# Kernel tuning notes

Measured on AMD Instinct MI355X. Metric: run time of the kernel, lower is better.

The kernel has to match this reference:

```python
import jax, jax.numpy as jnp
import numpy as np
import math

D_MODEL = 1024
N_HEADS = 16
HEAD_DIM = D_MODEL // N_HEADS


def setup_inputs() -> dict:
    key = jax.random.key(0)
    ks = jax.random.split(key, 6)
    scale = 1.0 / math.sqrt(D_MODEL)
    x = jax.random.normal(ks[0], (4, 2048, D_MODEL), dtype=jnp.float32)
    # nn.Linear weights stored as [out, in]; we keep [in, out] for x @ W
    Wq = jax.random.uniform(ks[1], (D_MODEL, D_MODEL), jnp.float32, -scale, scale)
    Wk = jax.random.uniform(ks[2], (D_MODEL, D_MODEL), jnp.float32, -scale, scale)
    Wv = jax.random.uniform(ks[3], (D_MODEL, D_MODEL), jnp.float32, -scale, scale)
    Wo = jax.random.uniform(ks[4], (D_MODEL, D_MODEL), jnp.float32, -scale, scale)
    bo = jax.random.uniform(ks[5], (D_MODEL,), jnp.float32, -scale, scale)
    return {"x": x, "Wq": Wq, "Wk": Wk, "Wv": Wv, "Wo": Wo, "bo": bo}


def reference(x, Wq, Wk, Wv, Wo, bo):
    B, S, _ = x.shape
    H, Dh = N_HEADS, HEAD_DIM
    # project and split heads -> [B, H, S, Dh]
    q = (x @ Wq).reshape(B, S, H, Dh).transpose(0, 2, 1, 3)
    k = (x @ Wk).reshape(B, S, H, Dh).transpose(0, 2, 1, 3)
    v = (x @ Wv).reshape(B, S, H, Dh).transpose(0, 2, 1, 3)
    scores = jnp.einsum('bhqd,bhkd->bhqk', q, k) / math.sqrt(Dh)
    causal = jnp.tril(jnp.ones((S, S), dtype=bool))  # True = keep
    scores = jnp.where(causal, scores, -jnp.inf)
    attn = jax.nn.softmax(scores, axis=-1)  # dropout=0.0 -> no-op
    out = jnp.einsum('bhqk,bhkd->bhqd', attn, v)
    out = out.transpose(0, 2, 1, 3).reshape(B, S, H * Dh)
    return out @ Wo + bo
```

## Files before the change

kernel.cpp:

```cpp
#include <hip/hip_runtime.h>
#include <hip/hip_bf16.h>

#define DEV __device__ __forceinline__

typedef unsigned short u16;
typedef unsigned int u32;
typedef __bf16 bf16x8 __attribute__((ext_vector_type(8)));
typedef float f32x4 __attribute__((ext_vector_type(4)));

static constexpr int S   = 2048;
static constexpr int D   = 1024;
static constexpr int H   = 16;
static constexpr int Dh  = 64;
static constexpr int B_  = 4;
static constexpr int M   = B_ * S;

DEV u16 f2bf(float f) {
    __hip_bfloat16 h = __float2bfloat16(f);
    union { __hip_bfloat16 h; u16 u; } cv; cv.h = h; return cv.u;
}
DEV float bf2f(u16 u) {
    union { u16 u; __hip_bfloat16 h; } cv; cv.u = u; return __bfloat162float(cv.h);
}
DEV f32x4 mfma16(bf16x8 a, bf16x8 b, f32x4 c) {
    return __builtin_amdgcn_mfma_f32_16x16x32_bf16(a, b, c, 0, 0, 0);
}
DEV void llds16(const u16* g, u16* l) {
    __builtin_amdgcn_global_load_lds(
        (const __attribute__((address_space(1))) u32*)g,
        (__attribute__((address_space(3))) u32*)l, 16, 0, 0);
}
DEV bf16x8 ld8f(const float* p) {
    const f32x4* q = reinterpret_cast<const f32x4*>(p);
    f32x4 a = q[0], b = q[1];
    union { u16 u[8]; bf16x8 v; } r;
    r.u[0] = f2bf(a[0]); r.u[1] = f2bf(a[1]); r.u[2] = f2bf(a[2]); r.u[3] = f2bf(a[3]);
    r.u[4] = f2bf(b[0]); r.u[5] = f2bf(b[1]); r.u[6] = f2bf(b[2]); r.u[7] = f2bf(b[3]);
    return r.v;
}

__global__ __launch_bounds__(256) void x_to_bf16(
    const float* __restrict__ x, u16* __restrict__ xb)
{
    size_t i = ((size_t)blockIdx.x * 256 + threadIdx.x) * 8;
    *reinterpret_cast<bf16x8*>(xb + i) = ld8f(x + i);
}

__global__ __launch_bounds__(256) void transpose_w(
    const float* __restrict__ Wq, const float* __restrict__ Wk,
    const float* __restrict__ Wv, const float* __restrict__ Wo,
    u16* __restrict__ WT)
{
    const float* src = blockIdx.z == 0 ? Wq : blockIdx.z == 1 ? Wk
                     : blockIdx.z == 2 ? Wv : Wo;
    u16* dst = WT + (size_t)blockIdx.z * D * D;
    __shared__ u16 T[64 * 72];
    const int k0 = blockIdx.x * 64, n0 = blockIdx.y * 64;
    const int tid = threadIdx.x;
    for (int c = tid; c < 512; c += 256) {
        int r = c >> 3, cc = (c & 7) << 3;
        *reinterpret_cast<bf16x8*>(&T[r * 72 + cc]) =
            ld8f(&src[(size_t)(k0 + r) * D + n0 + cc]);
    }
    __syncthreads();
    for (int c = tid; c < 512; c += 256) {
        int r = c >> 3, cc = (c & 7) << 3;
        u16 tmp[8];
        #pragma unroll
        for (int i = 0; i < 8; ++i) tmp[i] = T[(cc + i) * 72 + r];
        *reinterpret_cast<bf16x8*>(&dst[(size_t)(n0 + r) * D + k0 + cc]) =
            *reinterpret_cast<const bf16x8*>(tmp);
    }
}

__global__ __launch_bounds__(256) void qkv_gemm128(
    const u16* __restrict__ A, const u16* __restrict__ WT,
    u16* __restrict__ qkv, u16* __restrict__ vtb)
{
    const int bm = blockIdx.x;
    const int bn = blockIdx.y;

    __shared__ u16 As[128 * 32];
    __shared__ u16 Bs[128 * 32];
    __shared__ u16 Tt[64 * 136];

    const int tid  = threadIdx.x;
    const int wave = tid >> 6, ln = tid & 63;
    const int ln15 = ln & 15, quad = ln >> 4;
    const int wm = (wave >> 1) * 64, wn = (wave & 1) * 64;

    const u16* Ab = A  + (size_t)(bm * 128) * D;
    const u16* Bb = WT + (size_t)(bn * 128) * D;

    const int c0  = wave * 128 + ln;
    const int c1  = c0 + 64;
    const int r0  = c0 >> 2, o0 = (c0 & 3) * 8;
    const int r1  = c1 >> 2, o1 = (c1 & 3) * 8;

    f32x4 acc[4][4] = {};

    for (int k0 = 0; k0 < D; k0 += 32) {
        __syncthreads();
        llds16(Ab + (size_t)r0 * D + k0 + o0, &As[(wave * 2 + 0) * 512]);
        llds16(Ab + (size_t)r1 * D + k0 + o1, &As[(wave * 2 + 1) * 512]);
        llds16(Bb + (size_t)r0 * D + k0 + o0, &Bs[(wave * 2 + 0) * 512]);
        llds16(Bb + (size_t)r1 * D + k0 + o1, &Bs[(wave * 2 + 1) * 512]);
        __syncthreads();
        bf16x8 af[4], bfr[4];
        #pragma unroll
        for (int i = 0; i < 4; ++i)
            af[i] = *reinterpret_cast<const bf16x8*>(&As[(wm + i * 16 + ln15) * 32 + quad * 8]);
        #pragma unroll
        for (int j = 0; j < 4; ++j)
            bfr[j] = *reinterpret_cast<const bf16x8*>(&Bs[(wn + j * 16 + ln15) * 32 + quad * 8]);
        #pragma unroll
        for (int i = 0; i < 4; ++i)
            #pragma unroll
            for (int j = 0; j < 4; ++j)
                acc[i][j] = mfma16(af[i], bfr[j], acc[i][j]);
    }

    const int matn = bn >> 3;
    if (matn < 2) {
        u16* outp = qkv + (size_t)matn * M * D;
        #pragma unroll
        for (int i = 0; i < 4; ++i)
            #pragma unroll
            for (int j = 0; j < 4; ++j)
                #pragma unroll
                for (int r = 0; r < 4; ++r) {
                    int t = bm * 128 + wm + i * 16 + quad * 4 + r;
                    int b = t >> 11, s = t & (S - 1);
                    int n = (bn & 7) * 128 + wn + j * 16 + ln15;
                    int head = n >> 6, dh = n & 63;
                    outp[(((size_t)(b * H + head)) * S + s) * Dh + dh] = f2bf(acc[i][j][r]);
                }
    } else {
        const int t0 = bm * 128, b = t0 >> 11, s0 = t0 & (S - 1);
        #pragma unroll
        for (int h2 = 0; h2 < 2; ++h2) {
            __syncthreads();
            if ((wn == 0) == (h2 == 0)) {
                #pragma unroll
                for (int i = 0; i < 4; ++i)
                    #pragma unroll
                    for (int j = 0; j < 4; ++j)
                        #pragma unroll
                        for (int r = 0; r < 4; ++r) {
                            int sl = wm + i * 16 + quad * 4 + r;
                            int dh = j * 16 + ln15;
                            Tt[dh * 136 + sl] = f2bf(acc[i][j][r]);
                        }
            }
            __syncthreads();
            const int bh = b * H + (bn & 7) * 2 + h2;
            u16* dst = vtb + (size_t)bh * Dh * S + s0;
            for (int c = tid; c < 1024; c += 256) {
                int r = c >> 4, cc = (c & 15) * 8;
                *reinterpret_cast<bf16x8*>(&dst[(size_t)r * S + cc]) =
                    *reinterpret_cast<const bf16x8*>(&Tt[r * 136 + cc]);
            }
        }
    }
}

__global__ __launch_bounds__(256) void attn_kernel(
    const u16* __restrict__ qbuf, const u16* __restrict__ kbuf,
    const u16* __restrict__ vt, u16* __restrict__ attno)
{
    const int i  = blockIdx.x;
    const int bh = blockIdx.y;
    const int b = bh >> 4, h = bh & 15;
    const int qt[4] = {i, 15 - i, 16 + i, 31 - i};

    __shared__ u16 Ks[2][64 * 64];
    __shared__ u16 Vs[2][64 * 64];
    __shared__ u16 Ps[4][16 * 72];

    const int tid  = threadIdx.x;
    const int wave = tid >> 6, ln = tid & 63;
    const int ln15 = ln & 15, quad = ln >> 4;
    const int swz  = ln15 & 7;

    const u16* kp0 = kbuf + (size_t)bh * S * Dh;
    const u16* vp0 = vt   + (size_t)bh * Dh * S;

    bf16x8 qf[4][2];
    #pragma unroll
    for (int t = 0; t < 4; ++t) {
        const u16* qp = qbuf + ((size_t)bh * S + qt[t] * 64) * Dh;
        for (int c = tid; c < 512; c += 256) {
            int r = c >> 3, cc = (c & 7) << 3;
            *reinterpret_cast<bf16x8*>(&Ks[0][r * 64 + cc]) =
                *reinterpret_cast<const bf16x8*>(&qp[r * 64 + cc]);
        }
        __syncthreads();
        #pragma unroll
        for (int st = 0; st < 2; ++st) {
            union { bf16x8 v; u16 u[8]; } in, ot;
            in.v = *reinterpret_cast<const bf16x8*>(&Ks[0][(wave * 16 + ln15) * 64 + st * 32 + quad * 8]);
            #pragma unroll
            for (int k = 0; k < 8; ++k) ot.u[k] = f2bf(bf2f(in.u[k]) * 0.18033688f);
            qf[t][st] = ot.v;
        }
        __syncthreads();
    }

    float l_st[4][4] = {};
    f32x4 o_st[4][4] = {};

    u16* psw = &Ps[wave][0];
    const int lrow = wave * 16 + quad * 4;

    const int c0 = wave * 128 + ln;
    const int c1 = c0 + 64;
    const int kr0 = c0 >> 3, ko0 = (((c0 & 7) ^ (kr0 & 7)) * 8);
    const int kr1 = c1 >> 3, ko1 = (((c1 & 7) ^ (kr1 & 7)) * 8);

    auto stage = [&](int kblk, int buf) {
        llds16(kp0 + ((size_t)kblk * 64 + kr0) * Dh + ko0, &Ks[buf][(wave * 2 + 0) * 512]);
        llds16(kp0 + ((size_t)kblk * 64 + kr1) * Dh + ko1, &Ks[buf][(wave * 2 + 1) * 512]);
        llds16(vp0 + (size_t)kr0 * S + kblk * 64 + ko0,    &Vs[buf][(wave * 2 + 0) * 512]);
        llds16(vp0 + (size_t)kr1 * S + kblk * 64 + ko1,    &Vs[buf][(wave * 2 + 1) * 512]);
    };

    bf16x8 kf[2][4], vf[2][4];

    auto step = [&](int t, bool domask) {
        const bf16x8* qa = qf[t];
        float* l_r = l_st[t];
        f32x4* oa = o_st[t];
        f32x4 sf[4] = {};
        #pragma unroll
        for (int j = 0; j < 4; ++j) {
            sf[j] = mfma16(qa[0], kf[0][j], sf[j]);
            sf[j] = mfma16(qa[1], kf[1][j], sf[j]);
        }
        if (domask) {
            #pragma unroll
            for (int j = 0; j < 4; ++j) {
                int kg = j * 16 + ln15;
                #pragma unroll
                for (int r = 0; r < 4; ++r)
                    if (kg > lrow + r) sf[j][r] = -3e38f;
            }
        }
        #pragma unroll
        for (int j = 0; j < 4; ++j)
            #pragma unroll
            for (int r = 0; r < 4; ++r) {
                float p = exp2f(sf[j][r] - 24.0f);
                sf[j][r] = p;
                l_r[r] += p;
            }
        #pragma unroll
        for (int j = 0; j < 4; ++j)
            #pragma unroll
            for (int r = 0; r < 4; ++r)
                psw[(quad * 4 + r) * 72 + j * 16 + ln15] = f2bf(sf[j][r]);

        #pragma unroll
        for (int st = 0; st < 2; ++st) {
            bf16x8 pa = *reinterpret_cast<const bf16x8*>(&psw[ln15 * 72 + st * 32 + quad * 8]);
            #pragma unroll
            for (int jd = 0; jd < 4; ++jd)
                oa[jd] = mfma16(pa, vf[st][jd], oa[jd]);
        }
    };

    const int nstage = qt[3] + 1;
    stage(0, 0);
    int cur = 0;
    for (int kblk = 0; kblk < nstage; ++kblk) {
        __syncthreads();
        if (kblk + 1 < nstage) stage(kblk + 1, cur ^ 1);
        #pragma unroll
        for (int st = 0; st < 2; ++st)
            #pragma unroll
            for (int j = 0; j < 4; ++j) {
                kf[st][j] = *reinterpret_cast<const bf16x8*>(
                    &Ks[cur][(j * 16 + ln15) * 64 + ((st * 4 + quad) ^ swz) * 8]);
                vf[st][j] = *reinterpret_cast<const bf16x8*>(
                    &Vs[cur][(j * 16 + ln15) * 64 + ((st * 4 + quad) ^ swz) * 8]);
            }
        step(3, kblk == qt[3]);
        if (kblk <= qt[2]) step(2, kblk == qt[2]);
        if (kblk <= qt[1]) step(1, kblk == qt[1]);
        if (kblk <= qt[0]) step(0, kblk == qt[0]);
        cur ^= 1;
    }

    #pragma unroll
    for (int t = 0; t < 4; ++t) {
        float linv[4];
        #pragma unroll
        for (int r = 0; r < 4; ++r) {
            float l = l_st[t][r];
            l += __shfl_xor(l, 1, 64);
            l += __shfl_xor(l, 2, 64);
            l += __shfl_xor(l, 4, 64);
            l += __shfl_xor(l, 8, 64);
            linv[r] = 1.0f / l;
        }
        #pragma unroll
        for (int jd = 0; jd < 4; ++jd)
            #pragma unroll
            for (int r = 0; r < 4; ++r) {
                int qrow = qt[t] * 64 + wave * 16 + quad * 4 + r;
                size_t off = ((size_t)(b * S + qrow)) * D + h * Dh + jd * 16 + ln15;
                attno[off] = f2bf(o_st[t][jd][r] * linv[r]);
            }
    }
}

__global__ __launch_bounds__(256) void proj_gemm128(
    const u16* __restrict__ A, const u16* __restrict__ WoT,
    const float* __restrict__ bo, float* __restrict__ out)
{
    const int bm = blockIdx.x;
    const int bn = blockIdx.y;

    __shared__ u16 As[128 * 32];
    __shared__ u16 Bs[128 * 32];

    const int tid  = threadIdx.x;
    const int wave = tid >> 6, ln = tid & 63;
    const int ln15 = ln & 15, quad = ln >> 4;
    const int wm = (wave >> 1) * 64, wn = (wave & 1) * 64;

    const u16* Ab = A   + (size_t)(bm * 128) * D;
    const u16* Bb = WoT + (size_t)(bn * 128) * D;

    const int c0 = wave * 128 + ln;
    const int c1 = c0 + 64;
    const int r0 = c0 >> 2, o0 = (c0 & 3) * 8;
    const int r1 = c1 >> 2, o1 = (c1 & 3) * 8;

    f32x4 acc[4][4] = {};

    for (int k0 = 0; k0 < D; k0 += 32) {
        __syncthreads();
        llds16(Ab + (size_t)r0 * D + k0 + o0, &As[(wave * 2 + 0) * 512]);
        llds16(Ab + (size_t)r1 * D + k0 + o1, &As[(wave * 2 + 1) * 512]);
        llds16(Bb + (size_t)r0 * D + k0 + o0, &Bs[(wave * 2 + 0) * 512]);
        llds16(Bb + (size_t)r1 * D + k0 + o1, &Bs[(wave * 2 + 1) * 512]);
        __syncthreads();
        bf16x8 af[4], bfr[4];
        #pragma unroll
        for (int i = 0; i < 4; ++i)
            af[i] = *reinterpret_cast<const bf16x8*>(&As[(wm + i * 16 + ln15) * 32 + quad * 8]);
        #pragma unroll
        for (int j = 0; j < 4; ++j)
            bfr[j] = *reinterpret_cast<const bf16x8*>(&Bs[(wn + j * 16 + ln15) * 32 + quad * 8]);
        #pragma unroll
        for (int i = 0; i < 4; ++i)
            #pragma unroll
            for (int j = 0; j < 4; ++j)
                acc[i][j] = mfma16(af[i], bfr[j], acc[i][j]);
    }

    #pragma unroll
    for (int i = 0; i < 4; ++i)
        #pragma unroll
        for (int j = 0; j < 4; ++j)
            #pragma unroll
            for (int r = 0; r < 4; ++r) {
                int t   = bm * 128 + wm + i * 16 + quad * 4 + r;
                int col = bn * 128 + wn + j * 16 + ln15;
                out[(size_t)t * D + col] = acc[i][j][r] + bo[col];
            }
}

extern "C" void kernel_launch(void* const* d_in, const int* in_sizes, int n_in,
                              void* d_out, int out_size, void* d_ws, size_t ws_size,
                              hipStream_t stream) {
    const float* x  = (const float*)d_in[0];
    const float* Wq = (const float*)d_in[1];
    const float* Wk = (const float*)d_in[2];
    const float* Wv = (const float*)d_in[3];
    const float* Wo = (const float*)d_in[4];
    const float* bo = (const float*)d_in[5];
    float* out = (float*)d_out;
    u16* ws  = (u16*)d_ws;

    u16* WT   = ws;
    u16* xb   = WT + (size_t)4 * D * D;
    u16* qkvb = xb + (size_t)M * D;
    u16* kb   = qkvb + (size_t)M * D;
    u16* vtb  = qkvb + (size_t)2 * M * D;
    u16* attn = xb;

    x_to_bf16   <<<dim3(M * D / (256 * 8)), 256, 0, stream>>>(x, xb);
    transpose_w <<<dim3(16, 16, 4), 256, 0, stream>>>(Wq, Wk, Wv, Wo, WT);
    qkv_gemm128 <<<dim3(64, 24),    256, 0, stream>>>(xb, WT, qkvb, vtb);
    attn_kernel <<<dim3(8, 64),     256, 0, stream>>>(qkvb, kb, vtb, attn);
    proj_gemm128<<<dim3(64, 8),     256, 0, stream>>>(attn, WT + (size_t)3 * D * D, bo, out);
}
```

Baseline: 280.3 us.

## Split attention into two query tiles per block and stage Q/K stores via LDS

The attention kernel now gives each block two paired query tiles (i, 31-i) instead of four, which doubles the grid to 16x64 blocks for more parallelism and fewer registers per thread. The constant softmax offset is folded into the MFMA accumulator initial value, and the P tile in shared memory switches to an XOR-swizzled layout with no padding to avoid bank conflicts. In the QKV GEMM, Q/K outputs are staged through a shared LDS buffer so they can be written to global memory as vectorized 16-byte stores instead of scattered 2-byte stores, and the LDS arrays are aliased to cut shared memory use. In exchange, K/V tiles are loaded from global memory twice as often across blocks, and the GEMM epilogue needs extra barriers.

Measured after the change: 288.4 us. 2.9% more time.

```diff
diff --git a/kernel.cpp b/kernel.cpp
--- a/kernel.cpp
+++ b/kernel.cpp
@@ -80,9 +80,9 @@
     const int bm = blockIdx.x;
     const int bn = blockIdx.y;
 
-    __shared__ u16 As[128 * 32];
-    __shared__ u16 Bs[128 * 32];
-    __shared__ u16 Tt[64 * 136];
+    __shared__ u16 SB[64 * 136];
+    u16* As = SB;
+    u16* Bs = SB + 4096;
 
     const int tid  = threadIdx.x;
     const int wave = tid >> 6, ln = tid & 63;
@@ -121,26 +121,38 @@
     }
 
     const int matn = bn >> 3;
+    const int t0 = bm * 128, b = t0 >> 11, s0 = t0 & (S - 1);
+    __syncthreads();
+
     if (matn < 2) {
         u16* outp = qkv + (size_t)matn * M * D;
         #pragma unroll
-        for (int i = 0; i < 4; ++i)
-            #pragma unroll
-            for (int j = 0; j < 4; ++j)
+        for (int h2 = 0; h2 < 2; ++h2) {
+            if ((wave >> 1) == h2) {
                 #pragma unroll
-                for (int r = 0; r < 4; ++r) {
-                    int t = bm * 128 + wm + i * 16 + quad * 4 + r;
-                    int b = t >> 11, s = t & (S - 1);
-                    int n = (bn & 7) * 128 + wn + j * 16 + ln15;
-                    int head = n >> 6, dh = n & 63;
-                    outp[(((size_t)(b * H + head)) * S + s) * Dh + dh] = f2bf(acc[i][j][r]);
-                }
+                for (int i = 0; i < 4; ++i)
+                    #pragma unroll
+                    for (int j = 0; j < 4; ++j)
+                        #pragma unroll
+                        for (int r = 0; r < 4; ++r)
+                            SB[(i * 16 + quad * 4 + r) * 136 + wn + j * 16 + ln15] =
+                                f2bf(acc[i][j][r]);
+            }
+            __syncthreads();
+            for (int c = tid; c < 1024; c += 256) {
+                int r = c >> 4, cc = (c & 15) * 8;
+                int head = (bn & 7) * 2 + (cc >> 6);
+                int s = s0 + h2 * 64 + r;
+                *reinterpret_cast<bf16x8*>(
+                    &outp[(((size_t)(b * H + head)) * S + s) * Dh + (cc & 63)]) =
+                    *reinterpret_cast<const bf16x8*>(&SB[r * 136 + cc]);
+            }
+            __syncthreads();
+        }
     } else {
-        const int t0 = bm * 128, b = t0 >> 11, s0 = t0 & (S - 1);
         #pragma unroll
         for (int h2 = 0; h2 < 2; ++h2) {
-            __syncthreads();
-            if ((wn == 0) == (h2 == 0)) {
+            if ((wave & 1) == h2) {
                 #pragma unroll
                 for (int i = 0; i < 4; ++i)
                     #pragma unroll
@@ -149,7 +161,7 @@
                         for (int r = 0; r < 4; ++r) {
                             int sl = wm + i * 16 + quad * 4 + r;
                             int dh = j * 16 + ln15;
-                            Tt[dh * 136 + sl] = f2bf(acc[i][j][r]);
+                            SB[dh * 136 + sl] = f2bf(acc[i][j][r]);
                         }
             }
             __syncthreads();
@@ -158,8 +170,9 @@
             for (int c = tid; c < 1024; c += 256) {
                 int r = c >> 4, cc = (c & 15) * 8;
                 *reinterpret_cast<bf16x8*>(&dst[(size_t)r * S + cc]) =
-                    *reinterpret_cast<const bf16x8*>(&Tt[r * 136 + cc]);
-            }
+                    *reinterpret_cast<const bf16x8*>(&SB[r * 136 + cc]);
+            }
+            __syncthreads();
         }
     }
 }
@@ -171,11 +184,11 @@
     const int i  = blockIdx.x;
     const int bh = blockIdx.y;
     const int b = bh >> 4, h = bh & 15;
-    const int qt[4] = {i, 15 - i, 16 + i, 31 - i};
+    const int qt[2] = {i, 31 - i};
 
     __shared__ u16 Ks[2][64 * 64];
     __shared__ u16 Vs[2][64 * 64];
-    __shared__ u16 Ps[4][16 * 72];
+    __shared__ u16 Ps[4][16 * 64];
 
     const int tid  = threadIdx.x;
     const int wave = tid >> 6, ln = tid & 63;
@@ -185,9 +198,9 @@
     const u16* kp0 = kbuf + (size_t)bh * S * Dh;
     const u16* vp0 = vt   + (size_t)bh * Dh * S;
 
-    bf16x8 qf[4][2];
+    bf16x8 qf[2][2];
     #pragma unroll
-    for (int t = 0; t < 4; ++t) {
+    for (int t = 0; t < 2; ++t) {
         const u16* qp = qbuf + ((size_t)bh * S + qt[t] * 64) * Dh;
         for (int c = tid; c < 512; c += 256) {
             int r = c >> 3, cc = (c & 7) << 3;
@@ -206,8 +219,8 @@
         __syncthreads();
     }
 
-    float l_st[4][4] = {};
-    f32x4 o_st[4][4] = {};
+    float l_st[2][4] = {};
+    f32x4 o_st[2][4] = {};
 
     u16* psw = &Ps[wave][0];
     const int lrow = wave * 16 + quad * 4;
@@ -230,7 +243,8 @@
         const bf16x8* qa = qf[t];
         float* l_r = l_st[t];
         f32x4* oa = o_st[t];
-        f32x4 sf[4] = {};
+        const f32x4 minit = {-24.f, -24.f, -24.f, -24.f};
+        f32x4 sf[4] = {minit, minit, minit, minit};
         #pragma unroll
         for (int j = 0; j < 4; ++j) {
             sf[j] = mfma16(qa[0], kf[0][j], sf[j]);
@@ -249,26 +263,30 @@
         for (int j = 0; j < 4; ++j)
             #pragma unroll
             for (int r = 0; r < 4; ++r) {
-                float p = exp2f(sf[j][r] - 24.0f);
+                float p = exp2f(sf[j][r]);
                 sf[j][r] = p;
                 l_r[r] += p;
             }
         #pragma unroll
         for (int j = 0; j < 4; ++j)
             #pragma unroll
-            for (int r = 0; r < 4; ++r)
-                psw[(quad * 4 + r) * 72 + j * 16 + ln15] = f2bf(sf[j][r]);
+            for (int r = 0; r < 4; ++r) {
+                int q = quad * 4 + r;
+                int phys = ((j * 2 + (ln15 >> 3)) ^ (q & 7)) * 8 + (ln15 & 7);
+                psw[q * 64 + phys] = f2bf(sf[j][r]);
+            }
 
         #pragma unroll
         for (int st = 0; st < 2; ++st) {
-            bf16x8 pa = *reinterpret_cast<const bf16x8*>(&psw[ln15 * 72 + st * 32 + quad * 8]);
+            bf16x8 pa = *reinterpret_cast<const bf16x8*>(
+                &psw[ln15 * 64 + ((st * 4 + quad) ^ swz) * 8]);
             #pragma unroll
             for (int jd = 0; jd < 4; ++jd)
                 oa[jd] = mfma16(pa, vf[st][jd], oa[jd]);
         }
     };
 
-    const int nstage = qt[3] + 1;
+    const int nstage = qt[1] + 1;
     stage(0, 0);
     int cur = 0;
     for (int kblk = 0; kblk < nstage; ++kblk) {
@@ -283,15 +301,13 @@
                 vf[st][j] = *reinterpret_cast<const bf16x8*>(
                     &Vs[cur][(j * 16 + ln15) * 64 + ((st * 4 + quad) ^ swz) * 8]);
             }
-        step(3, kblk == qt[3]);
-        if (kblk <= qt[2]) step(2, kblk == qt[2]);
-        if (kblk <= qt[1]) step(1, kblk == qt[1]);
+        step(1, kblk == qt[1]);
         if (kblk <= qt[0]) step(0, kblk == qt[0]);
         cur ^= 1;
     }
 
     #pragma unroll
-    for (int t = 0; t < 4; ++t) {
+    for (int t = 0; t < 2; ++t) {
         float linv[4];
         #pragma unroll
         for (int r = 0; r < 4; ++r) {
@@ -393,6 +409,6 @@
     x_to_bf16   <<<dim3(M * D / (256 * 8)), 256, 0, stream>>>(x, xb);
     transpose_w <<<dim3(16, 16, 4), 256, 0, stream>>>(Wq, Wk, Wv, Wo, WT);
     qkv_gemm128 <<<dim3(64, 24),    256, 0, stream>>>(xb, WT, qkvb, vtb);
-    attn_kernel <<<dim3(8, 64),     256, 0, stream>>>(qkvb, kb, vtb, attn);
+    attn_kernel <<<dim3(16, 64),    256, 0, stream>>>(qkvb, kb, vtb, attn);
     proj_gemm128<<<dim3(64, 8),     256, 0, stream>>>(attn, WT + (size_t)3 * D * D, bo, out);
 }
```
